# Performance work log

Hardware: AMD Instinct MI355X
Metric: run time of the kernel (lower is better)

The kernel has to match this reference:

```python
import jax, jax.numpy as jnp
import numpy as np

# GDN (gated delta-rule) linear attention, prefill path, single packed sequence,
# no initial conv/ssm state.
NUM_K_HEADS = 16
NUM_V_HEADS = 32
HEAD_K_DIM = 128
HEAD_V_DIM = 128
HIDDEN = 2048
CONV_K = 4
EPS = 1e-6
K_TOTAL = NUM_K_HEADS * HEAD_K_DIM
V_TOTAL = NUM_V_HEADS * HEAD_V_DIM
QKV_TOTAL = 2 * K_TOTAL + V_TOTAL


def setup_inputs() -> dict:
    key = jax.random.key(0)
    ks = jax.random.split(key, 9)
    T = 2048
    s = 0.02
    return {
        "hidden_states": jax.random.normal(ks[0], (T, HIDDEN), jnp.float32),
        "in_proj_qkv_weight": s * jax.random.normal(ks[1], (QKV_TOTAL, HIDDEN), jnp.float32),
        "in_proj_z_weight": s * jax.random.normal(ks[2], (V_TOTAL, HIDDEN), jnp.float32),
        "in_proj_a_weight": s * jax.random.normal(ks[3], (NUM_V_HEADS, HIDDEN), jnp.float32),
        "in_proj_b_weight": s * jax.random.normal(ks[4], (NUM_V_HEADS, HIDDEN), jnp.float32),
        "conv1d_weight": 0.1 * jax.random.normal(ks[5], (QKV_TOTAL, CONV_K), jnp.float32),
        "out_proj_weight": s * jax.random.normal(ks[6], (HIDDEN, V_TOTAL), jnp.float32),
        "norm_weight": jnp.ones((HEAD_V_DIM,), jnp.float32),
        "A_log": jnp.log(jnp.linspace(1.0, 8.0, NUM_V_HEADS, dtype=jnp.float32)),
        "dt_bias": 0.5 * jax.random.normal(ks[7], (NUM_V_HEADS,), jnp.float32),
    }


def _causal_conv1d_silu(x, w):
    # x: [T, C], w: [C, K] depthwise causal conv + SiLU
    T = x.shape[0]
    K = w.shape[1]
    xp = jnp.pad(x, ((K - 1, 0), (0, 0)))
    y = xp[0:T] * w[:, 0]
    for j in range(1, K):  # small fixed K
        y = y + xp[j:j + T] * w[:, j]
    return jax.nn.silu(y)


def _l2norm(x):
    return x / jnp.sqrt(jnp.sum(x * x, axis=-1, keepdims=True) + EPS)


def _gdn_recurrence(q, k, v, g, beta, scale):
    # q,k: [T,Hv,Dk] (l2-normed, repeated over GQA groups), v: [T,Hv,Dv]
    # g,beta: [T,Hv]. State S: [Hv,Dk,Dv]. Gated delta rule:
    #   S <- exp(g)*S ; S <- S + k^T beta (v - k S) ; o = scale * q S
    Hv, Dk = q.shape[1], q.shape[2]
    Dv = v.shape[2]

    def step(S, inp):
        q_t, k_t, v_t, g_t, b_t = inp
        S = S * jnp.exp(g_t)[:, None, None]
        pred = jnp.einsum('hk,hkv->hv', k_t, S)
        delta = b_t[:, None] * (v_t - pred)
        S = S + jnp.einsum('hk,hv->hkv', k_t, delta)
        o = jnp.einsum('hk,hkv->hv', q_t * scale, S)
        return S, o

    S0 = jnp.zeros((Hv, Dk, Dv), q.dtype)
    _, o = jax.lax.scan(step, S0, (q, k, v, g, beta))
    return o  # [T,Hv,Dv]


def reference(hidden_states, in_proj_qkv_weight, in_proj_z_weight, in_proj_a_weight,
              in_proj_b_weight, conv1d_weight, out_proj_weight, norm_weight, A_log, dt_bias):
    T = hidden_states.shape[0]
    mixed = hidden_states @ in_proj_qkv_weight.T            # [T, QKV_TOTAL]
    z = hidden_states @ in_proj_z_weight.T                  # [T, V_TOTAL]
    a = hidden_states @ in_proj_a_weight.T                  # [T, Hv]
    b = hidden_states @ in_proj_b_weight.T                  # [T, Hv]

    mixed = _causal_conv1d_silu(mixed, conv1d_weight)

    q, k, v = jnp.split(mixed, [K_TOTAL, 2 * K_TOTAL], axis=-1)
    q = q.reshape(T, NUM_K_HEADS, HEAD_K_DIM)
    k = k.reshape(T, NUM_K_HEADS, HEAD_K_DIM)
    v = v.reshape(T, NUM_V_HEADS, HEAD_V_DIM)

    # qk l2-norm in kernel, GQA repeat to v heads
    q = _l2norm(q)
    k = _l2norm(k)
    ratio = NUM_V_HEADS // NUM_K_HEADS
    q = jnp.repeat(q, ratio, axis=1)
    k = jnp.repeat(k, ratio, axis=1)

    # fused_gdn_gating: g = -exp(A_log) * softplus(a + dt_bias); beta = sigmoid(b)
    g = -jnp.exp(A_log) * jax.nn.softplus(a + dt_bias)      # [T,Hv]
    beta = jax.nn.sigmoid(b)                                # [T,Hv]

    o = _gdn_recurrence(q, k, v, g, beta, HEAD_K_DIM ** -0.5)  # [T,Hv,Dv]

    # gated RMSNorm: rmsnorm(o) * norm_weight * silu(z)
    o = o * jax.lax.rsqrt(jnp.mean(o * o, axis=-1, keepdims=True) + EPS) * norm_weight
    o = o * jax.nn.silu(z.reshape(T, NUM_V_HEADS, HEAD_V_DIM))

    return o.reshape(T, -1) @ out_proj_weight.T             # [T, HIDDEN]
```

## Files before the change

### kernel.cpp

```cpp
#include <hip/hip_runtime.h>
#include <math.h>

#define T_SEQ     2048
#define HIDDEN_D  2048
#define NUM_KH    16
#define NUM_VH    32
#define HEAD_DIM  128
#define K_TOTAL   2048
#define V_TOTAL   4096
#define QKV_TOTAL 8192
#define EPS_F     1e-6f
#define CC        32
#define NCHUNK    (T_SEQ / CC)
#define NV        8

typedef __attribute__((ext_vector_type(4))) float f32x4;
typedef __attribute__((ext_vector_type(8))) short s16x8;
typedef __attribute__((ext_vector_type(8))) unsigned short u16x8;

__device__ __forceinline__ unsigned short f2bf(float f) {
    unsigned int u = __float_as_uint(f);
    u += 0x7FFFu + ((u >> 16) & 1u);
    return (unsigned short)(u >> 16);
}

__device__ __forceinline__ float bf2f(unsigned short h) {
    return __uint_as_float((unsigned int)h << 16);
}

__global__ __launch_bounds__(256) void cast_bf16_kernel(
    const float* __restrict__ src, unsigned short* __restrict__ dst, int n4)
{
    int idx = blockIdx.x * 256 + threadIdx.x;
    if (idx >= n4) return;
    float4 v = ((const float4*)src)[idx];
    ushort4 o;
    o.x = f2bf(v.x); o.y = f2bf(v.y); o.z = f2bf(v.z); o.w = f2bf(v.w);
    ((ushort4*)dst)[idx] = o;
}

__global__ __launch_bounds__(256) void cast3_kernel(
    const float* __restrict__ hs, const float* __restrict__ Wqkv,
    const float* __restrict__ Wz, unsigned short* __restrict__ hs_bf,
    unsigned short* __restrict__ Wqkv_bf, unsigned short* __restrict__ Wz_bf)
{
    int idx = blockIdx.x * 256 + threadIdx.x;
    const float* src; unsigned short* dst; int off;
    if (idx < 1048576)      { src = hs;   dst = hs_bf;   off = idx; }
    else if (idx < 5242880) { src = Wqkv; dst = Wqkv_bf; off = idx - 1048576; }
    else                    { src = Wz;   dst = Wz_bf;   off = idx - 5242880; }
    float4 v = ((const float4*)src)[off];
    ushort4 o;
    o.x = f2bf(v.x); o.y = f2bf(v.y); o.z = f2bf(v.z); o.w = f2bf(v.w);
    ((ushort4*)dst)[off] = o;
}

__global__ __launch_bounds__(256) void gemm_bt_bf16(
    const unsigned short* __restrict__ A, const unsigned short* __restrict__ B,
    float* __restrict__ C, int M, int N, int K)
{
    __shared__ unsigned short As[128 * 64];
    __shared__ unsigned short Bs[128 * 64];
    const int tid  = threadIdx.x;
    const int wave = tid >> 6;
    const int lane = tid & 63;

    const int nx  = N >> 7;
    const int nwg = nx * (M >> 7);
    const int bid = blockIdx.y * nx + blockIdx.x;
    const int cpx = nwg >> 3;
    const int swz = (bid & 7) * cpx + (bid >> 3);
    const int m0 = (swz / nx) * 128;
    const int n0 = (swz % nx) * 128;

    const int wm = (wave >> 1) * 64;
    const int wn = (wave & 1) * 64;

    f32x4 acc[4][4];
    f32x4 zero = {0.f, 0.f, 0.f, 0.f};
#pragma unroll
    for (int i = 0; i < 4; ++i)
#pragma unroll
        for (int j = 0; j < 4; ++j) acc[i][j] = zero;

    const int srow = lane >> 3;
    const int scol = (lane & 7) * 8;
    const int rm = lane & 15;
    const int koq = (lane >> 4) * 8;

    for (int kt = 0; kt < K; kt += 64) {
#pragma unroll
        for (int l = 0; l < 4; ++l) {
            const int r0 = wave * 32 + l * 8;
            const unsigned short* ga =
                A + (size_t)(m0 + r0 + srow) * K + kt + scol;
            const unsigned short* gb =
                B + (size_t)(n0 + r0 + srow) * K + kt + scol;
            __builtin_amdgcn_global_load_lds(
                (const __attribute__((address_space(1))) void*)ga,
                (__attribute__((address_space(3))) void*)&As[r0 * 64], 16, 0, 0);
            __builtin_amdgcn_global_load_lds(
                (const __attribute__((address_space(1))) void*)gb,
                (__attribute__((address_space(3))) void*)&Bs[r0 * 64], 16, 0, 0);
        }
        __syncthreads();

#pragma unroll
        for (int ks = 0; ks < 2; ++ks) {
            const int ko = ks * 32 + koq;
            s16x8 af[4], bfr[4];
#pragma unroll
            for (int i = 0; i < 4; ++i) {
                af[i]  = *(const s16x8*)&As[(wm + i * 16 + rm) * 64 + ko];
                bfr[i] = *(const s16x8*)&Bs[(wn + i * 16 + rm) * 64 + ko];
            }
#pragma unroll
            for (int i = 0; i < 4; ++i)
#pragma unroll
                for (int j = 0; j < 4; ++j)
                    acc[i][j] = __builtin_amdgcn_mfma_f32_16x16x32_bf16(
                        af[i], bfr[j], acc[i][j], 0, 0, 0);
        }
        __syncthreads();
    }

    const int cr = (lane >> 4) * 4;
    const int ccol = lane & 15;
#pragma unroll
    for (int i = 0; i < 4; ++i)
#pragma unroll
        for (int j = 0; j < 4; ++j) {
#pragma unroll
            for (int r = 0; r < 4; ++r)
                C[(size_t)(m0 + wm + i * 16 + cr + r) * N
                  + n0 + wn + j * 16 + ccol] = acc[i][j][r];
        }
}

__global__ __launch_bounds__(256) void gemm_nt_64(
    const float* __restrict__ A, const float* __restrict__ B,
    float* __restrict__ C, int M, int N, int K)
{
    __shared__ float As[16][68];
    __shared__ float Bs[16][68];
    const int tid = threadIdx.x;
    const int m0 = blockIdx.y * 64;
    const int n0 = blockIdx.x * 64;
    const int tm = tid >> 4;
    const int tn = tid & 15;
    const int lr = tid >> 2;
    const int lc = (tid & 3) * 4;

    float acc[4][4];
#pragma unroll
    for (int i = 0; i < 4; ++i)
#pragma unroll
        for (int j = 0; j < 4; ++j) acc[i][j] = 0.f;

    for (int kt = 0; kt < K; kt += 16) {
        float4 av = *(const float4*)(A + (size_t)(m0 + lr) * K + kt + lc);
        float4 bv = *(const float4*)(B + (size_t)(n0 + lr) * K + kt + lc);
        As[lc + 0][lr] = av.x; As[lc + 1][lr] = av.y;
        As[lc + 2][lr] = av.z; As[lc + 3][lr] = av.w;
        Bs[lc + 0][lr] = bv.x; Bs[lc + 1][lr] = bv.y;
        Bs[lc + 2][lr] = bv.z; Bs[lc + 3][lr] = bv.w;
        __syncthreads();
#pragma unroll
        for (int kk = 0; kk < 16; ++kk) {
            float4 a4 = *(const float4*)&As[kk][tm * 4];
            float4 b4 = *(const float4*)&Bs[kk][tn * 4];
            float a[4] = {a4.x, a4.y, a4.z, a4.w};
            float b[4] = {b4.x, b4.y, b4.z, b4.w};
#pragma unroll
            for (int i = 0; i < 4; ++i)
#pragma unroll
                for (int j = 0; j < 4; ++j)
                    acc[i][j] = fmaf(a[i], b[j], acc[i][j]);
        }
        __syncthreads();
    }
#pragma unroll
    for (int i = 0; i < 4; ++i) {
        float4 o = make_float4(acc[i][0], acc[i][1], acc[i][2], acc[i][3]);
        *(float4*)(C + (size_t)(m0 + tm * 4 + i) * N + n0 + tn * 4) = o;
    }
}

__global__ __launch_bounds__(256) void concat_ab_kernel(
    const float* __restrict__ Wa, const float* __restrict__ Wb,
    float* __restrict__ Wab)
{
    int idx = blockIdx.x * 256 + threadIdx.x;
    int half = 16384;
    const float* src = (idx < half) ? Wa : Wb;
    int off = (idx < half) ? idx : idx - half;
    ((float4*)Wab)[idx] = ((const float4*)src)[off];
}

__global__ __launch_bounds__(256) void gating_finalize_kernel(
    const float* __restrict__ ab, const float* __restrict__ A_log,
    const float* __restrict__ dt_bias, float* __restrict__ g,
    float* __restrict__ beta)
{
    int idx = blockIdx.x * 256 + threadIdx.x;
    int t = idx >> 5, h = idx & 31;
    float a = ab[t * 64 + h] + dt_bias[h];
    float b = ab[t * 64 + 32 + h];
    float sp = (a > 20.f) ? a : log1pf(expf(a));
    g[idx] = -expf(A_log[h]) * sp;
    beta[idx] = 1.f / (1.f + expf(-b));
}

__global__ __launch_bounds__(256) void conv_v_kernel(
    const float* __restrict__ mixed, const float* __restrict__ cw,
    float* __restrict__ vb)
{
    int idx = blockIdx.x * 256 + threadIdx.x;
    int c = idx & (V_TOTAL - 1);
    int t = idx >> 12;
    int ch = 2 * K_TOTAL + c;
    const float4 w = *(const float4*)(cw + (size_t)ch * 4);
    const float* base = mixed + (size_t)t * QKV_TOTAL + ch;
    float y = w.w * base[0];
    if (t >= 1) y = fmaf(w.z, base[-QKV_TOTAL], y);
    if (t >= 2) y = fmaf(w.y, base[-2 * QKV_TOTAL], y);
    if (t >= 3) y = fmaf(w.x, base[-3 * QKV_TOTAL], y);
    vb[idx] = y / (1.f + expf(-y));
}

__global__ __launch_bounds__(64) void convqk_l2_kernel(
    const float* __restrict__ mixed, const float* __restrict__ cw,
    unsigned short* __restrict__ qk_bf)
{
    const int row = blockIdx.x;
    const int t = row >> 5;
    const int r = row & 31;
    const int lane = threadIdx.x;
    const int c = r * HEAD_DIM + lane * 2;
    const float4 w0 = *(const float4*)(cw + (size_t)c * 4);
    const float4 w1 = *(const float4*)(cw + (size_t)(c + 1) * 4);
    const float* base = mixed + (size_t)t * QKV_TOTAL + c;
    float2 x0 = *(const float2*)base;
    float y0 = w0.w * x0.x, y1 = w1.w * x0.y;
    if (t >= 1) {
        float2 x = *(const float2*)(base - QKV_TOTAL);
        y0 = fmaf(w0.z, x.x, y0); y1 = fmaf(w1.z, x.y, y1);
    }
    if (t >= 2) {
        float2 x = *(const float2*)(base - 2 * QKV_TOTAL);
        y0 = fmaf(w0.y, x.x, y0); y1 = fmaf(w1.y, x.y, y1);
    }
    if (t >= 3) {
        float2 x = *(const float2*)(base - 3 * QKV_TOTAL);
        y0 = fmaf(w0.x, x.x, y0); y1 = fmaf(w1.x, x.y, y1);
    }
    y0 = y0 / (1.f + expf(-y0));
    y1 = y1 / (1.f + expf(-y1));
    float s = y0 * y0 + y1 * y1;
    for (int off = 32; off > 0; off >>= 1) s += __shfl_down(s, off);
    s = __shfl(s, 0);
    float inv = rsqrtf(s + EPS_F);
    unsigned short* qb = qk_bf + (size_t)t * 4096 + c;
    qb[0] = f2bf(y0 * inv);
    qb[1] = f2bf(y1 * inv);
}

__global__ __launch_bounds__(256) void gdn_p1(
    const unsigned short* __restrict__ qk_bf, const float* __restrict__ g,
    const float* __restrict__ beta, unsigned short* __restrict__ PTbuf,
    unsigned short* __restrict__ K2buf, float* __restrict__ lam_g,
    float* __restrict__ bet_g)
{
    __shared__ float Kn[CC][132];
    __shared__ float Qn[CC][132];
    __shared__ float Wm[CC][33];
    __shared__ float Tld[CC][36];
    __shared__ float Pm[CC][33];
    __shared__ float Trl[CC][33];
    __shared__ float cums[CC];
    __shared__ float betas[CC];
    __shared__ float rlS[CC];

    const int tid = threadIdx.x;
    const int h   = blockIdx.x;
    const int cix = blockIdx.y;
    const int t0  = cix * CC;
    const int kh  = h >> 1;
    const float scale = 0.08838834764831845f;
    const size_t mb = ((size_t)cix * NUM_VH + h);
    const size_t sb = mb * CC;

    if (tid < CC) {
        float x = g[(size_t)(t0 + tid) * NUM_VH + h];
        float bv = beta[(size_t)(t0 + tid) * NUM_VH + h];
#pragma unroll
        for (int off = 1; off < 32; off <<= 1) {
            float n = __shfl_up(x, off);
            if (tid >= off) x += n;
        }
        cums[tid] = x;
        betas[tid] = bv;
        float c31 = __shfl(x, 31);
        lam_g[sb + tid] = expf(x);
        bet_g[sb + tid] = bv;
        rlS[tid] = expf(c31 - x);
    }
#pragma unroll
    for (int p = 0; p < 2; ++p) {
        int idx = p * 256 + tid;
        int i = idx >> 4, ch = (idx & 15) * 8;
        const unsigned short* qr =
            qk_bf + (size_t)(t0 + i) * 4096 + kh * HEAD_DIM + ch;
        u16x8 q8 = *(const u16x8*)qr;
        u16x8 k8 = *(const u16x8*)(qr + K_TOTAL);
        float4 kf0, kf1, qf0, qf1;
        kf0.x = bf2f(k8[0]); kf0.y = bf2f(k8[1]);
        kf0.z = bf2f(k8[2]); kf0.w = bf2f(k8[3]);
        kf1.x = bf2f(k8[4]); kf1.y = bf2f(k8[5]);
        kf1.z = bf2f(k8[6]); kf1.w = bf2f(k8[7]);
        qf0.x = bf2f(q8[0]) * scale; qf0.y = bf2f(q8[1]) * scale;
        qf0.z = bf2f(q8[2]) * scale; qf0.w = bf2f(q8[3]) * scale;
        qf1.x = bf2f(q8[4]) * scale; qf1.y = bf2f(q8[5]) * scale;
        qf1.z = bf2f(q8[6]) * scale; qf1.w = bf2f(q8[7]) * scale;
        *(float4*)&Kn[i][ch]     = kf0;
        *(float4*)&Kn[i][ch + 4] = kf1;
        *(float4*)&Qn[i][ch]     = qf0;
        *(float4*)&Qn[i][ch + 4] = qf1;
    }
    __syncthreads();

    {
        const int i0 = (tid >> 4) * 2, j0 = (tid & 15) * 2;
        float wa[2][2] = {{0.f, 0.f}, {0.f, 0.f}};
        float pa[2][2] = {{0.f, 0.f}, {0.f, 0.f}};
        for (int k = 0; k < HEAD_DIM; k += 4) {
            float4 a0 = *(const float4*)&Kn[i0][k];
            float4 a1 = *(const float4*)&Kn[i0 + 1][k];
            float4 b0 = *(const float4*)&Kn[j0][k];
            float4 b1 = *(const float4*)&Kn[j0 + 1][k];
            float4 c0 = *(const float4*)&Qn[i0][k];
            float4 c1 = *(const float4*)&Qn[i0 + 1][k];
            const float* ap0 = (const float*)&a0;
            const float* ap1 = (const float*)&a1;
            const float* bp0 = (const float*)&b0;
            const float* bp1 = (const float*)&b1;
            const float* cp0 = (const float*)&c0;
            const float* cp1 = (const float*)&c1;
#pragma unroll
            for (int cc = 0; cc < 4; ++cc) {
                wa[0][0] = fmaf(ap0[cc], bp0[cc], wa[0][0]);
                wa[0][1] = fmaf(ap0[cc], bp1[cc], wa[0][1]);
                wa[1][0] = fmaf(ap1[cc], bp0[cc], wa[1][0]);
                wa[1][1] = fmaf(ap1[cc], bp1[cc], wa[1][1]);
                pa[0][0] = fmaf(cp0[cc], bp0[cc], pa[0][0]);
                pa[0][1] = fmaf(cp0[cc], bp1[cc], pa[0][1]);
                pa[1][0] = fmaf(cp1[cc], bp0[cc], pa[1][0]);
                pa[1][1] = fmaf(cp1[cc], bp1[cc], pa[1][1]);
            }
        }
#pragma unroll
        for (int di = 0; di < 2; ++di)
#pragma unroll
            for (int dj = 0; dj < 2; ++dj) {
                int i = i0 + di, j = j0 + dj;
                float rr = expf(fminf(cums[i] - cums[j], 0.f));
                Wm[i][j] = (j < i) ? betas[i] * rr * wa[di][dj] : 0.f;
                Pm[i][j] = (j <= i) ? rr * pa[di][dj] : 0.f;
            }
    }
    __syncthreads();

    {
        const int col = tid >> 3, tk = tid & 7;
        if (tk == 0) Tld[0][col] = (col == 0) ? 1.f : 0.f;
        for (int i = 1; i < CC; ++i) {
            float part = 0.f;
            for (int j = tk; j < i; j += 8)
                part = fmaf(Wm[i][j], Tld[j][col], part);
            part += __shfl_xor(part, 4);
            part += __shfl_xor(part, 2);
            part += __shfl_xor(part, 1);
            if (tk == 0) Tld[i][col] = ((i == col) ? 1.f : 0.f) - part;
        }
    }
    __syncthreads();

    {
        const int i = tid >> 3, j0 = (tid & 7) * 4;
        const float r = rlS[i];
#pragma unroll
        for (int e = 0; e < 4; ++e)
            Trl[i][j0 + e] = Tld[i][j0 + e] * r;
        float4 accp = {0.f, 0.f, 0.f, 0.f};
        for (int m = 0; m < CC; ++m) {
            float pv = Pm[i][m];
            float4 tv = *(const float4*)&Tld[m][j0];
            accp.x = fmaf(pv, tv.x, accp.x);
            accp.y = fmaf(pv, tv.y, accp.y);
            accp.z = fmaf(pv, tv.z, accp.z);
            accp.w = fmaf(pv, tv.w, accp.w);
        }
        ushort4 pt4;
        pt4.x = f2bf(accp.x); pt4.y = f2bf(accp.y);
        pt4.z = f2bf(accp.z); pt4.w = f2bf(accp.w);
        *(ushort4*)(PTbuf + mb * (CC * CC) + tid * 4) = pt4;
    }
    __syncthreads();

    {
        const int m0 = tid >> 3;
        const int q  = (tid & 7) * 4;
        float acc[4][4];
#pragma unroll
        for (int c = 0; c < 4; ++c)
#pragma unroll
            for (int e = 0; e < 4; ++e) acc[c][e] = 0.f;
        for (int j = 0; j < CC; ++j) {
            float t = Trl[j][m0];
#pragma unroll
            for (int c = 0; c < 4; ++c) {
                float4 a = *(const float4*)&Kn[j][q + 32 * c];
                acc[c][0] = fmaf(t, a.x, acc[c][0]);
                acc[c][1] = fmaf(t, a.y, acc[c][1]);
                acc[c][2] = fmaf(t, a.z, acc[c][2]);
                acc[c][3] = fmaf(t, a.w, acc[c][3]);
            }
        }
        unsigned short* kout =
            K2buf + mb * (CC * HEAD_DIM) + m0 * HEAD_DIM + q;
#pragma unroll
        for (int c = 0; c < 4; ++c) {
            ushort4 o4;
            o4.x = f2bf(acc[c][0]); o4.y = f2bf(acc[c][1]);
            o4.z = f2bf(acc[c][2]); o4.w = f2bf(acc[c][3]);
            *(ushort4*)(kout + 32 * c) = o4;
        }
    }
}

__global__ __launch_bounds__(256, 2) void gdn_p2(
    const float* __restrict__ vb, const unsigned short* __restrict__ qk_bf,
    const unsigned short* __restrict__ PTbuf,
    const unsigned short* __restrict__ K2buf, const float* __restrict__ lam_g,
    const float* __restrict__ bet_g, float* __restrict__ o)
{
    __shared__ unsigned short Kn[CC][128];
    __shared__ unsigned short Qn[CC][128];
    __shared__ unsigned short K2l[2][CC][128];
    __shared__ float PTl[2][CC][36];
    __shared__ float Sm[HEAD_DIM][NV + 2];
    __shared__ float Dl[CC][NV + 2];
    __shared__ float lamS[2][CC], betS[2][CC];

    const int tid = threadIdx.x;
    const int wv  = tid >> 6;
    const int ln  = tid & 63;
    const int h   = blockIdx.x >> 4;
    const int V0  = (blockIdx.x & 15) * NV;
    const int kh  = h >> 1;
    const float scale = 0.08838834764831845f;

    const int ri = tid >> 3;
    const int rn = (tid & 3) * 2;
    const int hh = (tid >> 2) & 1;
    const int rx2 = ri & 3;

    const int fk = (tid >> 3) * 4;
    const int sn = tid & 7;

    const int drow = ln >> 4;
    const int dc   = ln & 15;

#define DMA_KQ(T0)                                                            \
    {                                                                         \
        _Pragma("unroll")                                                     \
        for (int p = 0; p < 2; ++p) {                                         \
            const int i = p * 16 + wv * 4 + drow;                             \
            const int sc = 2 * ((dc >> 1) ^ (i & 3)) + (dc & 1);              \
            const unsigned short* sq = qk_bf + (size_t)((T0) + i) * 4096      \
                                       + kh * HEAD_DIM + sc * 8;              \
            __builtin_amdgcn_global_load_lds(                                 \
                (const __attribute__((address_space(1))) void*)(sq + K_TOTAL),\
                (__attribute__((address_space(3))) void*)                     \
                    &Kn[p * 16 + wv * 4][0], 16, 0, 0);                       \
            __builtin_amdgcn_global_load_lds(                                 \
                (const __attribute__((address_space(1))) void*)sq,            \
                (__attribute__((address_space(3))) void*)                     \
                    &Qn[p * 16 + wv * 4][0], 16, 0, 0);                       \
        }                                                                     \
    }

#define DMA_K2(MB, BUF)                                                       \
    {                                                                         \
        _Pragma("unroll")                                                     \
        for (int p = 0; p < 2; ++p) {                                         \
            const unsigned short* sk = K2buf + (MB) * (CC * HEAD_DIM)         \
                                       + p * 2048 + wv * 512 + ln * 8;        \
            __builtin_amdgcn_global_load_lds(                                 \
                (const __attribute__((address_space(1))) void*)sk,            \
                (__attribute__((address_space(3))) void*)                     \
                    &K2l[BUF][p * 16 + wv * 4][0], 16, 0, 0);                 \
        }                                                                     \
    }

#pragma unroll
    for (int c = 0; c < 4; ++c) Sm[fk + c][sn] = 0.f;

    DMA_KQ(0);
    DMA_K2((size_t)h, 0);
    {
        ushort4 pt0 = *(const ushort4*)(PTbuf + (size_t)h * (CC * CC) + tid * 4);
        float4 pf;
        pf.x = bf2f(pt0.x); pf.y = bf2f(pt0.y);
        pf.z = bf2f(pt0.z); pf.w = bf2f(pt0.w);
        *(float4*)&PTl[0][tid >> 3][(tid & 7) * 4] = pf;
        if (tid < CC) {
            lamS[0][tid] = lam_g[(size_t)h * CC + tid];
            betS[0][tid] = bet_g[(size_t)h * CC + tid];
        }
    }
    float2 vR = *(const float2*)(vb + (size_t)ri * V_TOTAL
                                 + h * HEAD_DIM + V0 + rn);

    int cur = 0;
    for (int cix = 0; cix < NCHUNK; ++cix) {
        const int t0 = cix * CC;
        __syncthreads();

        const float lam = lamS[cur][ri];
        const float bet = betS[cur][ri];
        float r1x = 0.f, r1y = 0.f, r2x = 0.f, r2y = 0.f;
#pragma unroll
        for (int kk = 0; kk < 8; ++kk) {
            const int pc = (2 * (kk ^ rx2) + hh) * 8;
            const int cl = kk * 16 + hh * 8;
            u16x8 kv = *(const u16x8*)&Kn[ri][pc];
            u16x8 qv = *(const u16x8*)&Qn[ri][pc];
#pragma unroll
            for (int c8 = 0; c8 < 8; ++c8) {
                float kf = bf2f(kv[c8]);
                float qf = bf2f(qv[c8]);
                float2 s = *(const float2*)&Sm[cl + c8][rn];
                r1x = fmaf(kf, s.x, r1x);
                r1y = fmaf(kf, s.y, r1y);
                r2x = fmaf(qf, s.x, r2x);
                r2y = fmaf(qf, s.y, r2y);
            }
        }
        r1x += __shfl_xor(r1x, 4);
        r1y += __shfl_xor(r1y, 4);
        r2x += __shfl_xor(r2x, 4);
        r2y += __shfl_xor(r2y, 4);
        {
            float dlx = bet * (vR.x - lam * r1x);
            float dly = bet * (vR.y - lam * r1y);
            if (hh == 0) { Dl[ri][rn] = dlx; Dl[ri][rn + 1] = dly; }
        }
        const float lsc = lam * scale;
        float ox = r2x * lsc, oy = r2y * lsc;
        __syncthreads();

        const int nxt = cur ^ 1;
        ushort4 ptN; float lamN = 0.f, betN = 0.f; float2 vN;
        const int more = (cix + 1 < NCHUNK);
        if (more) {
            const int t0n = t0 + CC;
            const size_t mbn = (size_t)(cix + 1) * NUM_VH + h;
            DMA_KQ(t0n);
            DMA_K2(mbn, nxt);
            ptN = *(const ushort4*)(PTbuf + mbn * (CC * CC) + tid * 4);
            if (tid < CC) {
                lamN = lam_g[mbn * CC + tid];
                betN = bet_g[mbn * CC + tid];
            }
            vN = *(const float2*)(vb + (size_t)(t0n + ri) * V_TOTAL
                                  + h * HEAD_DIM + V0 + rn);
        }

        {
            for (int j = 0; j < CC; ++j) {
                float p = PTl[cur][ri][j];
                float2 d = *(const float2*)&Dl[j][rn];
                ox = fmaf(p, d.x, ox);
                oy = fmaf(p, d.y, oy);
            }
            if (hh == 0)
                *(float2*)(o + (size_t)(t0 + ri) * V_TOTAL + h * HEAD_DIM + V0 + rn)
                    = make_float2(ox, oy);
        }

        {
            const float lamL = lamS[cur][CC - 1];
            float s0 = lamL * Sm[fk + 0][sn];
            float s1 = lamL * Sm[fk + 1][sn];
            float s2 = lamL * Sm[fk + 2][sn];
            float s3 = lamL * Sm[fk + 3][sn];
            for (int j = 0; j < CC; ++j) {
                ushort4 kk = *(const ushort4*)&K2l[cur][j][fk];
                float d = Dl[j][sn];
                s0 = fmaf(bf2f(kk.x), d, s0);
                s1 = fmaf(bf2f(kk.y), d, s1);
                s2 = fmaf(bf2f(kk.z), d, s2);
                s3 = fmaf(bf2f(kk.w), d, s3);
            }
            Sm[fk + 0][sn] = s0;
            Sm[fk + 1][sn] = s1;
            Sm[fk + 2][sn] = s2;
            Sm[fk + 3][sn] = s3;
        }

        if (more) {
            float4 pf;
            pf.x = bf2f(ptN.x); pf.y = bf2f(ptN.y);
            pf.z = bf2f(ptN.z); pf.w = bf2f(ptN.w);
            *(float4*)&PTl[nxt][tid >> 3][(tid & 7) * 4] = pf;
            if (tid < CC) { lamS[nxt][tid] = lamN; betS[nxt][tid] = betN; }
            vR = vN;
        }
        cur = nxt;
    }
#undef DMA_KQ
#undef DMA_K2
}

__global__ __launch_bounds__(64) void rmsnorm_gate_kernel(
    const float* __restrict__ o, const float* __restrict__ z,
    const float* __restrict__ nw, unsigned short* __restrict__ ob_bf)
{
    const int row = blockIdx.x;
    const float* p = o + (size_t)row * HEAD_DIM;
    const float* zp = z + (size_t)row * HEAD_DIM;
    const int lane = threadIdx.x;
    float2 v = *(const float2*)(p + lane * 2);
    float s = v.x * v.x + v.y * v.y;
    for (int off = 32; off > 0; off >>= 1) s += __shfl_down(s, off);
    s = __shfl(s, 0);
    float inv = rsqrtf(s * (1.f / HEAD_DIM) + EPS_F);
    float2 zv = *(const float2*)(zp + lane * 2);
    float2 wv = *(const float2*)(nw + lane * 2);
    v.x = v.x * inv * wv.x * (zv.x / (1.f + expf(-zv.x)));
    v.y = v.y * inv * wv.y * (zv.y / (1.f + expf(-zv.y)));
    unsigned short* q = ob_bf + (size_t)row * HEAD_DIM + lane * 2;
    q[0] = f2bf(v.x);
    q[1] = f2bf(v.y);
}

extern "C" void kernel_launch(void* const* d_in, const int* in_sizes, int n_in,
                              void* d_out, int out_size, void* d_ws,
                              size_t ws_size, hipStream_t stream)
{
    const float* hs    = (const float*)d_in[0];
    const float* Wqkv  = (const float*)d_in[1];
    const float* Wz    = (const float*)d_in[2];
    const float* Wa    = (const float*)d_in[3];
    const float* Wb    = (const float*)d_in[4];
    const float* cw    = (const float*)d_in[5];
    const float* Wout  = (const float*)d_in[6];
    const float* nw    = (const float*)d_in[7];
    const float* A_log = (const float*)d_in[8];
    const float* dtb   = (const float*)d_in[9];
    float* out = (float*)d_out;

    float* F     = (float*)d_ws;
    float* mixed = F;
    float* ob    = F;
    unsigned short* PTbuf = (unsigned short*)(F + (size_t)8388608);
    unsigned short* ob_bf = (unsigned short*)(F + (size_t)8388608);
    unsigned short* K2buf = (unsigned short*)(F + (size_t)9437184);
    float* lam_b = F + (size_t)13631488;
    float* bet_b = F + (size_t)13697024;
    unsigned short* hs_bf   = (unsigned short*)(F + (size_t)16777216);
    unsigned short* Wqkv_bf = (unsigned short*)(F + (size_t)18874368);
    float* vb = F + (size_t)16777216;
    unsigned short* qk_bf = (unsigned short*)(F + (size_t)25165824);
    unsigned short* Wz_bf   = (unsigned short*)(F + (size_t)27262976);
    float* Wab = F + (size_t)27262976;
    float* ab  = F + (size_t)27394048;
    float* zb  = F + (size_t)33554432;
    unsigned short* Wout_bf = (unsigned short*)(F + (size_t)37748736);
    float* gb = F + (size_t)41943040;
    float* bb = F + (size_t)42008576;

    cast3_kernel<<<7340032 / 256, 256, 0, stream>>>(
        hs, Wqkv, Wz, hs_bf, Wqkv_bf, Wz_bf);
    gemm_bt_bf16<<<dim3(QKV_TOTAL / 128, T_SEQ / 128), 256, 0, stream>>>(
        hs_bf, Wqkv_bf, mixed, T_SEQ, QKV_TOTAL, HIDDEN_D);
    gemm_bt_bf16<<<dim3(V_TOTAL / 128, T_SEQ / 128), 256, 0, stream>>>(
        hs_bf, Wz_bf, zb, T_SEQ, V_TOTAL, HIDDEN_D);
    concat_ab_kernel<<<32768 / 256, 256, 0, stream>>>(Wa, Wb, Wab);
    gemm_nt_64<<<dim3(1, T_SEQ / 64), 256, 0, stream>>>(
        hs, Wab, ab, T_SEQ, 64, HIDDEN_D);
    gating_finalize_kernel<<<(T_SEQ * NUM_VH) / 256, 256, 0, stream>>>(
        ab, A_log, dtb, gb, bb);
    conv_v_kernel<<<(T_SEQ * V_TOTAL) / 256, 256, 0, stream>>>(
        mixed, cw, vb);
    convqk_l2_kernel<<<T_SEQ * 32, 64, 0, stream>>>(mixed, cw, qk_bf);
    gdn_p1<<<dim3(NUM_VH, NCHUNK), 256, 0, stream>>>(
        qk_bf, gb, bb, PTbuf, K2buf, lam_b, bet_b);
    gdn_p2<<<NUM_VH * (HEAD_DIM / NV), 256, 0, stream>>>(
        vb, qk_bf, PTbuf, K2buf, lam_b, bet_b, ob);
    rmsnorm_gate_kernel<<<T_SEQ * NUM_VH, 64, 0, stream>>>(ob, zb, nw, ob_bf);
    cast_bf16_kernel<<<2097152 / 256, 256, 0, stream>>>(Wout, Wout_bf, 2097152);
    gemm_bt_bf16<<<dim3(HIDDEN_D / 128, T_SEQ / 128), 256, 0, stream>>>(
        ob_bf, Wout_bf, out, T_SEQ, HIDDEN_D, V_TOTAL);
}
```

Measured before the change: 919.2 us.

## Split GDN recurrence over more blocks with narrower value slices and direct loads

```diff
diff --git a/kernel.cpp b/kernel.cpp
--- a/kernel.cpp
+++ b/kernel.cpp
@@ -12,7 +12,7 @@
 #define EPS_F     1e-6f
 #define CC        32
 #define NCHUNK    (T_SEQ / CC)
-#define NV        8
+#define NV        4
 
 typedef __attribute__((ext_vector_type(4))) float f32x4;
 typedef __attribute__((ext_vector_type(8))) short s16x8;
@@ -438,7 +438,7 @@
     }
 }
 
-__global__ __launch_bounds__(256, 2) void gdn_p2(
+__global__ __launch_bounds__(256, 4) void gdn_p2(
     const float* __restrict__ vb, const unsigned short* __restrict__ qk_bf,
     const unsigned short* __restrict__ PTbuf,
     const unsigned short* __restrict__ K2buf, const float* __restrict__ lam_g,
@@ -447,26 +447,24 @@
     __shared__ unsigned short Kn[CC][128];
     __shared__ unsigned short Qn[CC][128];
     __shared__ unsigned short K2l[2][CC][128];
-    __shared__ float PTl[2][CC][36];
-    __shared__ float Sm[HEAD_DIM][NV + 2];
-    __shared__ float Dl[CC][NV + 2];
-    __shared__ float lamS[2][CC], betS[2][CC];
+    __shared__ float Sm[HEAD_DIM][6];
+    __shared__ float Dl[CC][6];
 
     const int tid = threadIdx.x;
     const int wv  = tid >> 6;
     const int ln  = tid & 63;
-    const int h   = blockIdx.x >> 4;
-    const int V0  = (blockIdx.x & 15) * NV;
+    const int h   = blockIdx.x >> 5;
+    const int V0  = (blockIdx.x & 31) * NV;
     const int kh  = h >> 1;
     const float scale = 0.08838834764831845f;
 
-    const int ri = tid >> 3;
-    const int rn = (tid & 3) * 2;
-    const int hh = (tid >> 2) & 1;
-    const int rx2 = ri & 3;
-
-    const int fk = (tid >> 3) * 4;
-    const int sn = tid & 7;
+    const int ri  = tid >> 3;
+    const int hh4 = (tid >> 1) & 3;
+    const int rn  = (tid & 1) * 2;
+    const int rx  = ri & 3;
+
+    const int sk = tid >> 2;
+    const int sn = tid & 3;
 
     const int drow = ln >> 4;
     const int dc   = ln & 15;
@@ -494,129 +492,111 @@
     {                                                                         \
         _Pragma("unroll")                                                     \
         for (int p = 0; p < 2; ++p) {                                         \
-            const unsigned short* sk = K2buf + (MB) * (CC * HEAD_DIM)         \
-                                       + p * 2048 + wv * 512 + ln * 8;        \
+            const unsigned short* sk2 = K2buf + (MB) * (CC * HEAD_DIM)        \
+                                        + p * 2048 + wv * 512 + ln * 8;       \
             __builtin_amdgcn_global_load_lds(                                 \
-                (const __attribute__((address_space(1))) void*)sk,            \
+                (const __attribute__((address_space(1))) void*)sk2,           \
                 (__attribute__((address_space(3))) void*)                     \
                     &K2l[BUF][p * 16 + wv * 4][0], 16, 0, 0);                 \
         }                                                                     \
     }
 
-#pragma unroll
-    for (int c = 0; c < 4; ++c) Sm[fk + c][sn] = 0.f;
+    Sm[2 * sk][sn] = 0.f;
+    Sm[2 * sk + 1][sn] = 0.f;
 
     DMA_KQ(0);
     DMA_K2((size_t)h, 0);
-    {
-        ushort4 pt0 = *(const ushort4*)(PTbuf + (size_t)h * (CC * CC) + tid * 4);
-        float4 pf;
-        pf.x = bf2f(pt0.x); pf.y = bf2f(pt0.y);
-        pf.z = bf2f(pt0.z); pf.w = bf2f(pt0.w);
-        *(float4*)&PTl[0][tid >> 3][(tid & 7) * 4] = pf;
-        if (tid < CC) {
-            lamS[0][tid] = lam_g[(size_t)h * CC + tid];
-            betS[0][tid] = bet_g[(size_t)h * CC + tid];
-        }
-    }
     float2 vR = *(const float2*)(vb + (size_t)ri * V_TOTAL
                                  + h * HEAD_DIM + V0 + rn);
 
     int cur = 0;
     for (int cix = 0; cix < NCHUNK; ++cix) {
         const int t0 = cix * CC;
+        const size_t mb = (size_t)cix * NUM_VH + h;
         __syncthreads();
 
-        const float lam = lamS[cur][ri];
-        const float bet = betS[cur][ri];
+        const float lam  = lam_g[mb * CC + ri];
+        const float bet  = bet_g[mb * CC + ri];
+        const float lamL = lam_g[mb * CC + CC - 1];
+        u16x8 pt = *(const u16x8*)(PTbuf + mb * (CC * CC) + ri * CC + hh4 * 8);
+
         float r1x = 0.f, r1y = 0.f, r2x = 0.f, r2y = 0.f;
 #pragma unroll
-        for (int kk = 0; kk < 8; ++kk) {
-            const int pc = (2 * (kk ^ rx2) + hh) * 8;
-            const int cl = kk * 16 + hh * 8;
+        for (int j = 0; j < 4; ++j) {
+            const int c  = 4 * j + hh4;
+            const int pc = (2 * ((c >> 1) ^ rx) + (c & 1)) * 8;
             u16x8 kv = *(const u16x8*)&Kn[ri][pc];
             u16x8 qv = *(const u16x8*)&Qn[ri][pc];
+            const int kb = c * 8;
 #pragma unroll
             for (int c8 = 0; c8 < 8; ++c8) {
                 float kf = bf2f(kv[c8]);
                 float qf = bf2f(qv[c8]);
-                float2 s = *(const float2*)&Sm[cl + c8][rn];
+                float2 s = *(const float2*)&Sm[kb + c8][rn];
                 r1x = fmaf(kf, s.x, r1x);
                 r1y = fmaf(kf, s.y, r1y);
                 r2x = fmaf(qf, s.x, r2x);
                 r2y = fmaf(qf, s.y, r2y);
             }
         }
-        r1x += __shfl_xor(r1x, 4);
-        r1y += __shfl_xor(r1y, 4);
-        r2x += __shfl_xor(r2x, 4);
-        r2y += __shfl_xor(r2y, 4);
+        r1x += __shfl_xor(r1x, 2); r1x += __shfl_xor(r1x, 4);
+        r1y += __shfl_xor(r1y, 2); r1y += __shfl_xor(r1y, 4);
+        r2x += __shfl_xor(r2x, 2); r2x += __shfl_xor(r2x, 4);
+        r2y += __shfl_xor(r2y, 2); r2y += __shfl_xor(r2y, 4);
         {
             float dlx = bet * (vR.x - lam * r1x);
             float dly = bet * (vR.y - lam * r1y);
-            if (hh == 0) { Dl[ri][rn] = dlx; Dl[ri][rn + 1] = dly; }
+            if (hh4 == 0) { Dl[ri][rn] = dlx; Dl[ri][rn + 1] = dly; }
         }
         const float lsc = lam * scale;
         float ox = r2x * lsc, oy = r2y * lsc;
         __syncthreads();
 
         const int nxt = cur ^ 1;
-        ushort4 ptN; float lamN = 0.f, betN = 0.f; float2 vN;
+        float2 vN;
         const int more = (cix + 1 < NCHUNK);
         if (more) {
             const int t0n = t0 + CC;
-            const size_t mbn = (size_t)(cix + 1) * NUM_VH + h;
+            const size_t mbn = mb + NUM_VH;
             DMA_KQ(t0n);
             DMA_K2(mbn, nxt);
-            ptN = *(const ushort4*)(PTbuf + mbn * (CC * CC) + tid * 4);
-            if (tid < CC) {
-                lamN = lam_g[mbn * CC + tid];
-                betN = bet_g[mbn * CC + tid];
-            }
             vN = *(const float2*)(vb + (size_t)(t0n + ri) * V_TOTAL
                                   + h * HEAD_DIM + V0 + rn);
         }
 
         {
-            for (int j = 0; j < CC; ++j) {
-                float p = PTl[cur][ri][j];
+            float pox = 0.f, poy = 0.f;
+#pragma unroll
+            for (int jj = 0; jj < 8; ++jj) {
+                const int j = hh4 * 8 + jj;
+                float p = bf2f(pt[jj]);
                 float2 d = *(const float2*)&Dl[j][rn];
-                ox = fmaf(p, d.x, ox);
-                oy = fmaf(p, d.y, oy);
+                pox = fmaf(p, d.x, pox);
+                poy = fmaf(p, d.y, poy);
             }
-            if (hh == 0)
+            pox += __shfl_xor(pox, 2); pox += __shfl_xor(pox, 4);
+            poy += __shfl_xor(poy, 2); poy += __shfl_xor(poy, 4);
+            ox += pox; oy += poy;
+            if (hh4 == 0)
                 *(float2*)(o + (size_t)(t0 + ri) * V_TOTAL + h * HEAD_DIM + V0 + rn)
                     = make_float2(ox, oy);
         }
 
         {
-            const float lamL = lamS[cur][CC - 1];
-            float s0 = lamL * Sm[fk + 0][sn];
-            float s1 = lamL * Sm[fk + 1][sn];
-            float s2 = lamL * Sm[fk + 2][sn];
-            float s3 = lamL * Sm[fk + 3][sn];
+            float s0 = lamL * Sm[2 * sk][sn];
+            float s1 = lamL * Sm[2 * sk + 1][sn];
             for (int j = 0; j < CC; ++j) {
-                ushort4 kk = *(const ushort4*)&K2l[cur][j][fk];
+                unsigned int kk2 =
+                    *(const unsigned int*)&K2l[cur][j][2 * sk];
                 float d = Dl[j][sn];
-                s0 = fmaf(bf2f(kk.x), d, s0);
-                s1 = fmaf(bf2f(kk.y), d, s1);
-                s2 = fmaf(bf2f(kk.z), d, s2);
-                s3 = fmaf(bf2f(kk.w), d, s3);
+                s0 = fmaf(bf2f((unsigned short)(kk2 & 0xffffu)), d, s0);
+                s1 = fmaf(bf2f((unsigned short)(kk2 >> 16)), d, s1);
             }
-            Sm[fk + 0][sn] = s0;
-            Sm[fk + 1][sn] = s1;
-            Sm[fk + 2][sn] = s2;
-            Sm[fk + 3][sn] = s3;
-        }
-
-        if (more) {
-            float4 pf;
-            pf.x = bf2f(ptN.x); pf.y = bf2f(ptN.y);
-            pf.z = bf2f(ptN.z); pf.w = bf2f(ptN.w);
-            *(float4*)&PTl[nxt][tid >> 3][(tid & 7) * 4] = pf;
-            if (tid < CC) { lamS[nxt][tid] = lamN; betS[nxt][tid] = betN; }
-            vR = vN;
-        }
+            Sm[2 * sk][sn] = s0;
+            Sm[2 * sk + 1][sn] = s1;
+        }
+
+        if (more) vR = vN;
         cur = nxt;
     }
 #undef DMA_KQ
```

New measurement: 996.3 us. 8.4% more time.
